# Kernel optimization log

Measured on AMD Instinct MI355X. Metric: run time of the kernel, lower is better.

Reference implementation:

```python
import jax, jax.numpy as jnp
import numpy as np

NUM_CHANNELS = 4096  # fill_max for ch_ids; all ids appear w.h.p. since batch >> channels


def setup_inputs() -> dict:
    key = jax.random.key(0)
    k1, k2, k3 = jax.random.split(key, 3)
    B, D = 524288, 128
    z = jax.random.normal(k1, (B, D), dtype=jnp.float32)
    y = jax.random.randint(k2, (B,), 0, 2, dtype=jnp.int64)
    ch_ids = jax.random.randint(k3, (B,), 0, NUM_CHANNELS, dtype=jnp.int64)
    return {"z": z, "y": y, "ch_ids": ch_ids}


def reference(z, y, ch_ids):
    # Segment-mean of z over channel ids, plus first-occurrence label per channel.
    C = NUM_CHANNELS
    B = z.shape[0]
    seg = ch_ids.astype(jnp.int32)
    # sum and count per channel in a single pass each (scatter-add)
    z_sum = jax.ops.segment_sum(z, seg, num_segments=C)              # (C, D)
    cnt = jax.ops.segment_sum(jnp.ones((B,), z.dtype), seg, num_segments=C)  # (C,)
    z_ch = z_sum / jnp.maximum(cnt, 1.0)[:, None]  # mean reduction
    # label of first window in each channel: scatter-min of row indices, then gather
    first_idx = jnp.full((C,), B, dtype=jnp.int32).at[seg].min(jnp.arange(B, dtype=jnp.int32))
    y_ch = y[jnp.minimum(first_idx, B - 1)]
    return z_ch, y_ch
```

## Files before the change

kernel.cpp:

```cpp
#include <hip/hip_runtime.h>

#define C_CH 4096
#define D_DIM 128
#define CAP   256

typedef float f32x2 __attribute__((ext_vector_type(2)));

__global__ __launch_bounds__(256) void init_cursor(int* cursor) {
    int i = blockIdx.x * blockDim.x + threadIdx.x;
    if (i < C_CH) cursor[i] = i * CAP;
}

__global__ __launch_bounds__(256) void scatter_kernel(const int* __restrict__ ids,
                                                      int* __restrict__ cursor,
                                                      int* __restrict__ order, int B) {
    int t = blockIdx.x * blockDim.x + threadIdx.x;
    int row = t * 4;
    if (row + 3 < B) {
        int4 v = ((const int4*)ids)[t];
        int p0 = atomicAdd(&cursor[v.x], 1);
        int p1 = atomicAdd(&cursor[v.y], 1);
        int p2 = atomicAdd(&cursor[v.z], 1);
        int p3 = atomicAdd(&cursor[v.w], 1);
        order[p0] = row + 0;
        order[p1] = row + 1;
        order[p2] = row + 2;
        order[p3] = row + 3;
    } else {
        for (int k = 0; k < 4; ++k)
            if (row + k < B) { int pos = atomicAdd(&cursor[ids[row + k]], 1); order[pos] = row + k; }
    }
}

__global__ __launch_bounds__(256) void reduce_kernel(
        const float* __restrict__ z, const int* __restrict__ order,
        const int* __restrict__ cursor, const int* __restrict__ y,
        float* __restrict__ out, int B) {
    int w = blockIdx.x * 4 + (threadIdx.x >> 6);
    int lane = threadIdx.x & 63;
    int beg = w * CAP;
    int end = cursor[w];
    const f32x2* z2 = (const f32x2*)z;

    f32x2 a0 = {0.f, 0.f}, a1 = {0.f, 0.f}, a2 = {0.f, 0.f}, a3 = {0.f, 0.f};
    f32x2 a4 = {0.f, 0.f}, a5 = {0.f, 0.f}, a6 = {0.f, 0.f}, a7 = {0.f, 0.f};
    int mn = B - 1;

    if (end > beg) {
        for (int r = beg; r < end; r += 16) {
            int idx[16];
            #pragma unroll
            for (int k = 0; k < 16; ++k)
                idx[k] = order[min(r + k, end - 1)];
            f32x2 v[16];
            #pragma unroll
            for (int k = 0; k < 16; ++k)
                v[k] = __builtin_nontemporal_load(&z2[(size_t)idx[k] * 64 + lane]);
            #pragma unroll
            for (int k = 0; k < 16; ++k) {
                mn = min(mn, idx[k]);
                if (r + k < end) {
                    switch (k & 7) {
                        case 0: a0 += v[k]; break;
                        case 1: a1 += v[k]; break;
                        case 2: a2 += v[k]; break;
                        case 3: a3 += v[k]; break;
                        case 4: a4 += v[k]; break;
                        case 5: a5 += v[k]; break;
                        case 6: a6 += v[k]; break;
                        case 7: a7 += v[k]; break;
                    }
                }
            }
        }
    }
    f32x2 sum = ((a0 + a1) + (a2 + a3)) + ((a4 + a5) + (a6 + a7));
    int cnt_c = end - beg;
    float inv = 1.f / (float)max(cnt_c, 1);
    f32x2 res; res.x = sum.x * inv; res.y = sum.y * inv;
    ((f32x2*)out)[(size_t)w * 64 + lane] = res;
    if (lane == 0) {
        out[(size_t)C_CH * D_DIM + w] = (float)y[mn];
    }
}

extern "C" void kernel_launch(void* const* d_in, const int* in_sizes, int n_in,
                              void* d_out, int out_size, void* d_ws, size_t ws_size,
                              hipStream_t stream) {
    const float* z   = (const float*)d_in[0];
    const int*   y   = (const int*)d_in[1];
    const int*   ids = (const int*)d_in[2];
    float* out = (float*)d_out;
    const int B = in_sizes[2];

    int* cursor = (int*)d_ws;
    int* order  = cursor + C_CH;

    init_cursor<<<(C_CH + 255) / 256, 256, 0, stream>>>(cursor);
    int tquads = (B + 3) / 4;
    scatter_kernel<<<(tquads + 255) / 256, 256, 0, stream>>>(ids, cursor, order, B);
    reduce_kernel<<<C_CH / 4, 256, 0, stream>>>(z, order, cursor, y, out, B);
}
```

Baseline: 383.8 us.

## Split each channel reduction across two waves with 16-byte loads and LDS index staging

The reduce kernel now gives each channel two wavefronts instead of one. Each half-wave loads 16-byte float4 vectors, so one wave covers two rows per load instruction. The channel's row indices are first staged into shared memory, and the partial sums are combined with a cross-half shuffle and then a shared-memory exchange between the two waves. The aim is more memory-level parallelism and wider loads for the gather-bound reduction, at the cost of extra syncs and shared memory per block.

```diff
diff --git a/kernel.cpp b/kernel.cpp
--- a/kernel.cpp
+++ b/kernel.cpp
@@ -4,7 +4,7 @@
 #define D_DIM 128
 #define CAP   256
 
-typedef float f32x2 __attribute__((ext_vector_type(2)));
+typedef float f32x4 __attribute__((ext_vector_type(4)));
 
 __global__ __launch_bounds__(256) void init_cursor(int* cursor) {
     int i = blockIdx.x * blockDim.x + threadIdx.x;
@@ -36,51 +36,78 @@
         const float* __restrict__ z, const int* __restrict__ order,
         const int* __restrict__ cursor, const int* __restrict__ y,
         float* __restrict__ out, int B) {
-    int w = blockIdx.x * 4 + (threadIdx.x >> 6);
-    int lane = threadIdx.x & 63;
-    int beg = w * CAP;
-    int end = cursor[w];
-    const f32x2* z2 = (const f32x2*)z;
+    __shared__ int   lidx[2][CAP];
+    __shared__ float lacc[2][D_DIM];
+    __shared__ int   lmn[2];
 
-    f32x2 a0 = {0.f, 0.f}, a1 = {0.f, 0.f}, a2 = {0.f, 0.f}, a3 = {0.f, 0.f};
-    f32x2 a4 = {0.f, 0.f}, a5 = {0.f, 0.f}, a6 = {0.f, 0.f}, a7 = {0.f, 0.f};
+    int tid  = threadIdx.x;
+    int chl  = tid >> 7;
+    int c    = blockIdx.x * 2 + chl;
+    int s    = (tid >> 6) & 1;
+    int lane = tid & 63;
+    int h    = lane >> 5;
+    int sl   = lane & 31;
+    int beg  = c * CAP;
+    int cnt  = cursor[c] - beg;
+
+    int i = tid & 127;
+    if (i < cnt)       lidx[chl][i]       = order[beg + i];
+    if (i + 128 < cnt) lidx[chl][i + 128] = order[beg + 128 + i];
+    __syncthreads();
+
+    const f32x4* z4 = (const f32x4*)z;
+    f32x4 a0 = {0,0,0,0}, a1 = {0,0,0,0}, a2 = {0,0,0,0}, a3 = {0,0,0,0};
     int mn = B - 1;
 
-    if (end > beg) {
-        for (int r = beg; r < end; r += 16) {
-            int idx[16];
-            #pragma unroll
-            for (int k = 0; k < 16; ++k)
-                idx[k] = order[min(r + k, end - 1)];
-            f32x2 v[16];
-            #pragma unroll
-            for (int k = 0; k < 16; ++k)
-                v[k] = __builtin_nontemporal_load(&z2[(size_t)idx[k] * 64 + lane]);
-            #pragma unroll
-            for (int k = 0; k < 16; ++k) {
-                mn = min(mn, idx[k]);
-                if (r + k < end) {
-                    switch (k & 7) {
-                        case 0: a0 += v[k]; break;
-                        case 1: a1 += v[k]; break;
-                        case 2: a2 += v[k]; break;
-                        case 3: a3 += v[k]; break;
-                        case 4: a4 += v[k]; break;
-                        case 5: a5 += v[k]; break;
-                        case 6: a6 += v[k]; break;
-                        case 7: a7 += v[k]; break;
-                    }
+    for (int r0 = s * 16; r0 < cnt; r0 += 32) {
+        int slot[8];
+        #pragma unroll
+        for (int k = 0; k < 8; ++k) {
+            int rs = r0 + 2 * k + h;
+            slot[k] = lidx[chl][min(rs, cnt - 1)];
+        }
+        f32x4 v[8];
+        #pragma unroll
+        for (int k = 0; k < 8; ++k)
+            v[k] = __builtin_nontemporal_load(&z4[(size_t)slot[k] * 32 + sl]);
+        #pragma unroll
+        for (int k = 0; k < 8; ++k) {
+            mn = min(mn, slot[k]);
+            int rs = r0 + 2 * k + h;
+            if (rs < cnt) {
+                switch (k & 3) {
+                    case 0: a0 += v[k]; break;
+                    case 1: a1 += v[k]; break;
+                    case 2: a2 += v[k]; break;
+                    case 3: a3 += v[k]; break;
                 }
             }
         }
     }
-    f32x2 sum = ((a0 + a1) + (a2 + a3)) + ((a4 + a5) + (a6 + a7));
-    int cnt_c = end - beg;
-    float inv = 1.f / (float)max(cnt_c, 1);
-    f32x2 res; res.x = sum.x * inv; res.y = sum.y * inv;
-    ((f32x2*)out)[(size_t)w * 64 + lane] = res;
-    if (lane == 0) {
-        out[(size_t)C_CH * D_DIM + w] = (float)y[mn];
+    f32x4 acc = (a0 + a1) + (a2 + a3);
+
+    acc.x += __shfl_xor(acc.x, 32);
+    acc.y += __shfl_xor(acc.y, 32);
+    acc.z += __shfl_xor(acc.z, 32);
+    acc.w += __shfl_xor(acc.w, 32);
+    mn = min(mn, __shfl_xor(mn, 32));
+
+    if (s == 1) {
+        if (h == 0) *(f32x4*)&lacc[chl][4 * sl] = acc;
+        if (lane == 0) lmn[chl] = mn;
+    }
+    __syncthreads();
+    if (s == 0) {
+        if (h == 0) {
+            f32x4 o = acc + *(const f32x4*)&lacc[chl][4 * sl];
+            float inv = 1.f / (float)max(cnt, 1);
+            o.x *= inv; o.y *= inv; o.z *= inv; o.w *= inv;
+            ((f32x4*)out)[(size_t)c * 32 + sl] = o;
+        }
+        if (lane == 0) {
+            int m2 = min(mn, lmn[chl]);
+            out[(size_t)C_CH * D_DIM + c] = (float)y[m2];
+        }
     }
 }
 
@@ -99,5 +126,5 @@
     init_cursor<<<(C_CH + 255) / 256, 256, 0, stream>>>(cursor);
     int tquads = (B + 3) / 4;
     scatter_kernel<<<(tquads + 255) / 256, 256, 0, stream>>>(ids, cursor, order, B);
-    reduce_kernel<<<C_CH / 4, 256, 0, stream>>>(z, order, cursor, y, out, B);
+    reduce_kernel<<<C_CH / 2, 256, 0, stream>>>(z, order, cursor, y, out, B);
 }
```

Result: no change. 378.0 us (-1.5%).

## Replace bucket-sort gather with LDS-atomic privatized segment sums per column slab

Applied to the files above, without the earlier changes.

Replaces the atomic bucketing of row indices plus the gather reduction with a privatized histogram. Each of 256 blocks owns one 8-column slice of D and one row slab, and accumulates into a 4096x9 float LDS array using workgroup-scope float atomics. A final kernel then sums the 16 slab partials, divides by the counts, and looks up the first-occurrence label recorded by a global atomicMin. This streams z contiguously instead of doing random row gathers, but it depends on LDS atomic contention and on the extra partial-sum writes and reads. The cap of 256 rows per channel is also removed.

```diff
diff --git a/kernel.cpp b/kernel.cpp
--- a/kernel.cpp
+++ b/kernel.cpp
@@ -1,86 +1,97 @@
 #include <hip/hip_runtime.h>
 
-#define C_CH 4096
-#define D_DIM 128
-#define CAP   256
+#define C_CH   4096
+#define D_DIM  128
+#define NSLAB  16
+#define NJ     16
+#define ACC_W  9
+#define AB_THREADS 1024
 
-typedef float f32x2 __attribute__((ext_vector_type(2)));
+typedef float f32x4 __attribute__((ext_vector_type(4)));
 
-__global__ __launch_bounds__(256) void init_cursor(int* cursor) {
-    int i = blockIdx.x * blockDim.x + threadIdx.x;
-    if (i < C_CH) cursor[i] = i * CAP;
+static __device__ __forceinline__ void lds_fadd(float* p, float v) {
+    __hip_atomic_fetch_add(p, v, __ATOMIC_RELAXED, __HIP_MEMORY_SCOPE_WORKGROUP);
 }
 
-__global__ __launch_bounds__(256) void scatter_kernel(const int* __restrict__ ids,
-                                                      int* __restrict__ cursor,
-                                                      int* __restrict__ order, int B) {
-    int t = blockIdx.x * blockDim.x + threadIdx.x;
-    int row = t * 4;
-    if (row + 3 < B) {
-        int4 v = ((const int4*)ids)[t];
-        int p0 = atomicAdd(&cursor[v.x], 1);
-        int p1 = atomicAdd(&cursor[v.y], 1);
-        int p2 = atomicAdd(&cursor[v.z], 1);
-        int p3 = atomicAdd(&cursor[v.w], 1);
-        order[p0] = row + 0;
-        order[p1] = row + 1;
-        order[p2] = row + 2;
-        order[p3] = row + 3;
-    } else {
-        for (int k = 0; k < 4; ++k)
-            if (row + k < B) { int pos = atomicAdd(&cursor[ids[row + k]], 1); order[pos] = row + k; }
+__global__ __launch_bounds__(256) void init_first(int* first) {
+    int i = blockIdx.x * blockDim.x + threadIdx.x;
+    if (i < C_CH) first[i] = 0x7fffffff;
+}
+
+__global__ __launch_bounds__(AB_THREADS, 1) void accum_kernel(
+        const float* __restrict__ z, const int* __restrict__ ids,
+        float* __restrict__ Psum, float* __restrict__ Pcnt,
+        int* __restrict__ first, int B) {
+    extern __shared__ float acc[];
+    int bi   = blockIdx.x;
+    int slab = bi & (NSLAB - 1);
+    int j    = bi >> 4;
+    int t    = threadIdx.x;
+
+    for (int i = t; i < C_CH * ACC_W; i += AB_THREADS) acc[i] = 0.f;
+    __syncthreads();
+
+    int rows = (B + NSLAB - 1) / NSLAB;
+    int beg  = slab * rows;
+    int end  = min(beg + rows, B);
+    int rr   = t >> 1;
+    int hh   = t & 1;
+    const f32x4* z4 = (const f32x4*)z;
+    bool track = (j == 0) && (hh == 0);
+
+    for (int r0 = beg; r0 < end; r0 += AB_THREADS / 2) {
+        int r = r0 + rr;
+        if (r < end) {
+            int c = ids[r];
+            f32x4 v = z4[(size_t)r * 32 + j * 2 + hh];
+            float* a = &acc[c * ACC_W + hh * 4];
+            lds_fadd(&a[0], v.x);
+            lds_fadd(&a[1], v.y);
+            lds_fadd(&a[2], v.z);
+            lds_fadd(&a[3], v.w);
+            if (track) {
+                lds_fadd(&acc[c * ACC_W + 8], 1.0f);
+                atomicMin(&first[c], r);
+            }
+        }
+    }
+    __syncthreads();
+
+    float* P = Psum + (size_t)bi * (C_CH * 8);
+    for (int i = t; i < C_CH * 8; i += AB_THREADS) {
+        int c = i >> 3, dl = i & 7;
+        P[i] = acc[c * ACC_W + dl];
+    }
+    if (j == 0) {
+        float* Q = Pcnt + (size_t)slab * C_CH;
+        for (int c = t; c < C_CH; c += AB_THREADS) Q[c] = acc[c * ACC_W + 8];
     }
 }
 
-__global__ __launch_bounds__(256) void reduce_kernel(
-        const float* __restrict__ z, const int* __restrict__ order,
-        const int* __restrict__ cursor, const int* __restrict__ y,
+__global__ __launch_bounds__(256) void final_kernel(
+        const float* __restrict__ Psum, const float* __restrict__ Pcnt,
+        const int* __restrict__ first, const int* __restrict__ y,
         float* __restrict__ out, int B) {
-    int w = blockIdx.x * 4 + (threadIdx.x >> 6);
-    int lane = threadIdx.x & 63;
-    int beg = w * CAP;
-    int end = cursor[w];
-    const f32x2* z2 = (const f32x2*)z;
+    int cbase = blockIdx.x * 32;
+    int t  = threadIdx.x;
+    int c  = cbase + (t >> 3);
+    int dl = t & 7;
 
-    f32x2 a0 = {0.f, 0.f}, a1 = {0.f, 0.f}, a2 = {0.f, 0.f}, a3 = {0.f, 0.f};
-    f32x2 a4 = {0.f, 0.f}, a5 = {0.f, 0.f}, a6 = {0.f, 0.f}, a7 = {0.f, 0.f};
-    int mn = B - 1;
+    float cnt = 0.f;
+    for (int s = 0; s < NSLAB; ++s) cnt += Pcnt[s * C_CH + c];
+    float inv = 1.f / fmaxf(cnt, 1.f);
 
-    if (end > beg) {
-        for (int r = beg; r < end; r += 16) {
-            int idx[16];
-            #pragma unroll
-            for (int k = 0; k < 16; ++k)
-                idx[k] = order[min(r + k, end - 1)];
-            f32x2 v[16];
-            #pragma unroll
-            for (int k = 0; k < 16; ++k)
-                v[k] = __builtin_nontemporal_load(&z2[(size_t)idx[k] * 64 + lane]);
-            #pragma unroll
-            for (int k = 0; k < 16; ++k) {
-                mn = min(mn, idx[k]);
-                if (r + k < end) {
-                    switch (k & 7) {
-                        case 0: a0 += v[k]; break;
-                        case 1: a1 += v[k]; break;
-                        case 2: a2 += v[k]; break;
-                        case 3: a3 += v[k]; break;
-                        case 4: a4 += v[k]; break;
-                        case 5: a5 += v[k]; break;
-                        case 6: a6 += v[k]; break;
-                        case 7: a7 += v[k]; break;
-                    }
-                }
-            }
-        }
+    for (int jj = 0; jj < NJ; ++jj) {
+        float sum = 0.f;
+        #pragma unroll
+        for (int s = 0; s < NSLAB; ++s)
+            sum += Psum[(size_t)(jj * NSLAB + s) * (C_CH * 8) + (size_t)c * 8 + dl];
+        out[(size_t)c * D_DIM + jj * 8 + dl] = sum * inv;
     }
-    f32x2 sum = ((a0 + a1) + (a2 + a3)) + ((a4 + a5) + (a6 + a7));
-    int cnt_c = end - beg;
-    float inv = 1.f / (float)max(cnt_c, 1);
-    f32x2 res; res.x = sum.x * inv; res.y = sum.y * inv;
-    ((f32x2*)out)[(size_t)w * 64 + lane] = res;
-    if (lane == 0) {
-        out[(size_t)C_CH * D_DIM + w] = (float)y[mn];
+    if (t < 32) {
+        int c2 = cbase + t;
+        int fi = min(first[c2], B - 1);
+        out[(size_t)C_CH * D_DIM + c2] = (float)y[fi];
     }
 }
 
@@ -93,11 +104,20 @@
     float* out = (float*)d_out;
     const int B = in_sizes[2];
 
-    int* cursor = (int*)d_ws;
-    int* order  = cursor + C_CH;
+    int*   first = (int*)d_ws;
+    float* Pcnt  = (float*)(first + C_CH);
+    float* Psum  = Pcnt + NSLAB * C_CH;
 
-    init_cursor<<<(C_CH + 255) / 256, 256, 0, stream>>>(cursor);
-    int tquads = (B + 3) / 4;
-    scatter_kernel<<<(tquads + 255) / 256, 256, 0, stream>>>(ids, cursor, order, B);
-    reduce_kernel<<<C_CH / 4, 256, 0, stream>>>(z, order, cursor, y, out, B);
+    static bool attr_done = false;
+    if (!attr_done) {
+        (void)hipFuncSetAttribute((const void*)accum_kernel,
+                                  hipFuncAttributeMaxDynamicSharedMemorySize,
+                                  C_CH * ACC_W * (int)sizeof(float));
+        attr_done = true;
+    }
+
+    init_first<<<(C_CH + 255) / 256, 256, 0, stream>>>(first);
+    accum_kernel<<<NJ * NSLAB, AB_THREADS, C_CH * ACC_W * sizeof(float), stream>>>(
+        z, ids, Psum, Pcnt, first, B);
+    final_kernel<<<C_CH / 32, 256, 0, stream>>>(Psum, Pcnt, first, y, out, B);
 }
```

Measured after the change: 651.1 us. +69.7%, slower.
